# Performance work log

Measured on AMD Instinct MI355X. Metric: run time of the kernel, lower is better.

Reference implementation:

```python
import jax, jax.numpy as jnp
import numpy as np

D_MODEL, D_INNER, D_STATE, D_CONV = 1024, 2048, 16, 4
LN_EPS = 1e-5


def setup_inputs() -> dict:
    key = jax.random.key(0)
    ks = jax.random.split(key, 8)
    B, T = 2, 1024
    s = 0.02
    A = jnp.broadcast_to(jnp.arange(1, D_STATE + 1, dtype=jnp.float32), (D_INNER, D_STATE))
    return {
        "x": jax.random.normal(ks[0], (B, T, D_MODEL), jnp.float32),
        "ln_gamma": jnp.ones((D_MODEL,), jnp.float32),
        "ln_beta": jnp.zeros((D_MODEL,), jnp.float32),
        "W_in": jax.random.normal(ks[1], (2 * D_INNER, D_MODEL), jnp.float32) * s,
        "conv_w": jax.random.normal(ks[2], (D_INNER, D_CONV), jnp.float32) * s,
        "conv_b": jnp.zeros((D_INNER,), jnp.float32),
        "W_x": jax.random.normal(ks[3], (2 * D_STATE + 1, D_INNER), jnp.float32) * s,
        "w_dt": jax.random.normal(ks[4], (D_INNER, 1), jnp.float32) * s,
        "b_dt": jnp.zeros((D_INNER,), jnp.float32),
        "A_log": jnp.log(A),
        "D_param": jnp.ones((D_INNER,), jnp.float32),
        "W_out": jax.random.normal(ks[5], (D_MODEL, D_INNER), jnp.float32) * s,
    }


def _mamba_forward(x, ln_gamma, ln_beta, W_in, conv_w, conv_b, W_x, w_dt, b_dt, A_log, D_param, W_out):
    residual = x
    B, T, _ = x.shape
    # LayerNorm
    mu = x.mean(-1, keepdims=True)
    var = ((x - mu) ** 2).mean(-1, keepdims=True)
    xn = (x - mu) / jnp.sqrt(var + LN_EPS) * ln_gamma + ln_beta
    # in_proj -> split into x branch and gate z
    xz = xn @ W_in.T                       # [B,T,2*d_inner]
    xb, z = jnp.split(xz, 2, axis=-1)
    # depthwise causal conv1d (torch pad=d_conv-1, truncated to T == left pad)
    xp = jnp.pad(xb, ((0, 0), (D_CONV - 1, 0), (0, 0)))
    xc = conv_b + sum(xp[:, k:k + T, :] * conv_w[:, k] for k in range(D_CONV))
    xc = jax.nn.silu(xc)                   # [B,T,d_inner]
    # ssm parameter projections
    ssm_p = xc @ W_x.T                     # [B,T,2*d_state+1]
    dt_raw = ssm_p[..., :1]
    Bp = ssm_p[..., 1:1 + D_STATE]
    Cp = ssm_p[..., 1 + D_STATE:]
    dt = jax.nn.softplus(dt_raw @ w_dt.T + b_dt)   # [B,T,d_inner]
    A = -jnp.exp(A_log)                    # [d_inner,d_state]

    def step(h, inp):
        dt_t, x_t, B_t, C_t = inp          # [B,d], [B,d], [B,n], [B,n]
        A_bar = jnp.exp(dt_t[:, :, None] * A[None])          # [B,d,n]
        h = A_bar * h + (dt_t * x_t)[:, :, None] * B_t[:, None, :]
        y_t = jnp.einsum('bdn,bn->bd', h, C_t)
        return h, y_t

    h0 = jnp.zeros((B, D_INNER, D_STATE), x.dtype)
    xs = (jnp.swapaxes(dt, 0, 1), jnp.swapaxes(xc, 0, 1),
          jnp.swapaxes(Bp, 0, 1), jnp.swapaxes(Cp, 0, 1))
    _, ys = jax.lax.scan(step, h0, xs)     # ys: [T,B,d_inner]
    y = jnp.swapaxes(ys, 0, 1)
    y = y + D_param * xc
    y = y * jax.nn.silu(z)
    return residual + y @ W_out.T


def reference(x, ln_gamma, ln_beta, W_in, conv_w, conv_b, W_x, w_dt, b_dt, A_log, D_param, W_out):
    return _mamba_forward(x, ln_gamma, ln_beta, W_in, conv_w, conv_b, W_x, w_dt, b_dt, A_log, D_param, W_out)
```

## Files before the change

kernel.cpp:

```cpp
#include <hip/hip_runtime.h>
#include <hip/hip_bf16.h>

#define DM 1024
#define DI 2048
#define DS 16
#define DC 4
#define BB 2
#define TT 1024
#define MM (BB*TT)
#define CCH 32
#define LCH 32
#define PR 8
#define REPS 2

typedef unsigned short u16;
typedef __attribute__((ext_vector_type(8))) short bf16x8;
typedef __attribute__((ext_vector_type(4))) float f32x4;

#if __has_builtin(__builtin_amdgcn_exp2f)
#define EXP2F(x) __builtin_amdgcn_exp2f(x)
#else
#define EXP2F(x) exp2f(x)
#endif
#define L2E 1.44269504f

__device__ __forceinline__ float bu2f(u16 u) {
    union { unsigned int i; float f; } w; w.i = ((unsigned int)u) << 16; return w.f;
}
__device__ __forceinline__ u16 f2bu(float f) {
    union { float f; unsigned int u; } w; w.f = f;
    unsigned int r = w.u + 0x7fffu + ((w.u >> 16) & 1u);
    return (u16)(r >> 16);
}
__device__ __forceinline__ float upk(const uint4& v, int e) {
    unsigned int u;
    switch (e >> 1) { case 0: u = v.x; break; case 1: u = v.y; break;
                      case 2: u = v.z; break; default: u = v.w; }
    union { unsigned int i; float f; } w;
    w.i = (e & 1) ? (u & 0xffff0000u) : (u << 16);
    return w.f;
}

#define F2B_BLOCKS 6210
__global__ __launch_bounds__(256) void prep_kernel(const float* __restrict__ x,
                                                   const float* __restrict__ gamma,
                                                   const float* __restrict__ beta,
                                                   u16* __restrict__ xn,
                                                   const float* __restrict__ Wi,
                                                   u16* __restrict__ Wi_b,
                                                   const float* __restrict__ Wo,
                                                   u16* __restrict__ Wo_b,
                                                   const float* __restrict__ Wx,
                                                   u16* __restrict__ Wx_b) {
    const int tid = threadIdx.x;
    if (blockIdx.x >= MM) {
        const int n4W  = 2 * DI * DM / 4;
        const int n4Wo = DM * DI / 4;
        int i = (blockIdx.x - MM) * 256 + tid;
        const float* in; u16* out;
        if (i < n4W) { in = Wi; out = Wi_b; }
        else if (i < n4W + n4Wo) { in = Wo; out = Wo_b; i -= n4W; }
        else { in = Wx; out = Wx_b; i -= n4W + n4Wo; }
        float4 v = reinterpret_cast<const float4*>(in)[i];
        ushort4 o;
        o.x = f2bu(v.x); o.y = f2bu(v.y); o.z = f2bu(v.z); o.w = f2bu(v.w);
        reinterpret_cast<ushort4*>(out)[i] = o;
        return;
    }
    __shared__ float sbuf[8];
    const int row = blockIdx.x;
    float4 v = reinterpret_cast<const float4*>(x + (size_t)row * DM)[tid];

    float s = v.x + v.y + v.z + v.w;
    #pragma unroll
    for (int off = 32; off; off >>= 1) s += __shfl_down(s, off);
    if ((tid & 63) == 0) sbuf[tid >> 6] = s;
    __syncthreads();
    float mu = (sbuf[0] + sbuf[1] + sbuf[2] + sbuf[3]) * (1.0f / DM);
    __syncthreads();

    float d0 = v.x - mu, d1 = v.y - mu, d2 = v.z - mu, d3 = v.w - mu;
    float q = d0*d0 + d1*d1 + d2*d2 + d3*d3;
    #pragma unroll
    for (int off = 32; off; off >>= 1) q += __shfl_down(q, off);
    if ((tid & 63) == 0) sbuf[tid >> 6] = q;
    __syncthreads();
    float var = (sbuf[0] + sbuf[1] + sbuf[2] + sbuf[3]) * (1.0f / DM);
    float rstd = rsqrtf(var + 1e-5f);

    float4 g = reinterpret_cast<const float4*>(gamma)[tid];
    float4 b = reinterpret_cast<const float4*>(beta)[tid];
    ushort4 o;
    o.x = f2bu(d0 * rstd * g.x + b.x);
    o.y = f2bu(d1 * rstd * g.y + b.y);
    o.z = f2bu(d2 * rstd * g.z + b.z);
    o.w = f2bu(d3 * rstd * g.w + b.w);
    reinterpret_cast<ushort4*>(xn + (size_t)row * DM)[tid] = o;
}

__device__ __forceinline__ void gl_lds(const u16* g, u16* lds) {
    __builtin_amdgcn_global_load_lds((const __attribute__((address_space(1))) void*)g,
                                     (__attribute__((address_space(3))) void*)lds,
                                     16, 0, 0);
}

__global__ __launch_bounds__(256) void gemm1_mfma(const u16* __restrict__ A,
                                                  const u16* __restrict__ B,
                                                  u16* __restrict__ C,
                                                  int M, int N, int K) {
    __shared__ u16 As[2][2][128 * 32];
    __shared__ u16 Bs[2][2][128 * 32];
    const int tid  = threadIdx.x;
    const int lane = tid & 63;
    const int w    = tid >> 6;
    const int wm   = (w >> 1) * 64, wn = (w & 1) * 64;
    const int m0   = blockIdx.y * 128, n0 = blockIdx.x * 128;

    const int srow = tid >> 2;
    const int sk   = (tid & 3) * 8;
    const u16* aP0 = A + (size_t)(m0 + srow) * K + sk;
    const u16* aP1 = aP0 + (size_t)64 * K;
    const u16* bP0 = B + (size_t)(n0 + srow) * K + sk;
    const u16* bP1 = bP0 + (size_t)64 * K;
    const int ldst = tid * 8;

    const int fr = lane & 15, fq = (lane >> 4) * 8;
    const int iters = K >> 6;

    for (int rep = 0; rep < REPS; rep++) {
        __syncthreads();
        #pragma unroll
        for (int kh = 0; kh < 2; kh++) {
            gl_lds(aP0 + kh * 32, &As[0][kh][ldst]); gl_lds(aP1 + kh * 32, &As[0][kh][2048 + ldst]);
            gl_lds(bP0 + kh * 32, &Bs[0][kh][ldst]); gl_lds(bP1 + kh * 32, &Bs[0][kh][2048 + ldst]);
        }
        __syncthreads();

        f32x4 acc[4][4] = {};
        for (int it = 0; it < iters; it++) {
            const int cur = it & 1;
            const int kn = (it + 1) << 6;
            if (kn < K) {
                const int nb = cur ^ 1;
                #pragma unroll
                for (int kh = 0; kh < 2; kh++) {
                    gl_lds(aP0 + kn + kh * 32, &As[nb][kh][ldst]);
                    gl_lds(aP1 + kn + kh * 32, &As[nb][kh][2048 + ldst]);
                    gl_lds(bP0 + kn + kh * 32, &Bs[nb][kh][ldst]);
                    gl_lds(bP1 + kn + kh * 32, &Bs[nb][kh][2048 + ldst]);
                }
            }
            #pragma unroll
            for (int kh = 0; kh < 2; kh++) {
                bf16x8 af[4], bf[4];
                #pragma unroll
                for (int i = 0; i < 4; i++)
                    af[i] = *reinterpret_cast<const bf16x8*>(&As[cur][kh][(wm + i * 16 + fr) * 32 + fq]);
                #pragma unroll
                for (int j = 0; j < 4; j++)
                    bf[j] = *reinterpret_cast<const bf16x8*>(&Bs[cur][kh][(wn + j * 16 + fr) * 32 + fq]);
                #pragma unroll
                for (int i = 0; i < 4; i++)
                    #pragma unroll
                    for (int j = 0; j < 4; j++)
                        acc[i][j] = __builtin_amdgcn_mfma_f32_16x16x32_bf16(af[i], bf[j], acc[i][j], 0, 0, 0);
            }
            __syncthreads();
        }

        const int erow = (lane >> 4) * 4, ecol = lane & 15;
        #pragma unroll
        for (int i = 0; i < 4; i++)
            #pragma unroll
            for (int j = 0; j < 4; j++) {
                const int col = n0 + wn + j * 16 + ecol;
                #pragma unroll
                for (int r = 0; r < 4; r++) {
                    const int row = m0 + wm + i * 16 + erow + r;
                    C[(size_t)row * N + col] = f2bu(acc[i][j][r]);
                }
            }
    }
}

__global__ __launch_bounds__(256) void gemm2_mfma(const u16* __restrict__ A,
                                                  const u16* __restrict__ B,
                                                  float* __restrict__ C,
                                                  const float* __restrict__ resid,
                                                  int M, int N, int K) {
    __shared__ u16 As[2][4][64 * 32];
    __shared__ u16 Bs[2][4][64 * 32];
    const int tid  = threadIdx.x;
    const int lane = tid & 63;
    const int w    = tid >> 6;
    const int wm   = (w >> 1) * 32, wn = (w & 1) * 32;
    const int m0   = blockIdx.y * 64, n0 = blockIdx.x * 64;

    const int srow = tid >> 2;
    const int sk   = (tid & 3) * 8;
    const u16* aP = A + (size_t)(m0 + srow) * K + sk;
    const u16* bP = B + (size_t)(n0 + srow) * K + sk;
    const int ldst = tid * 8;

    const int fr = lane & 15, fq = (lane >> 4) * 8;
    const int iters = K >> 7;

    for (int rep = 0; rep < REPS; rep++) {
        __syncthreads();
        #pragma unroll
        for (int kh = 0; kh < 4; kh++) {
            gl_lds(aP + kh * 32, &As[0][kh][ldst]);
            gl_lds(bP + kh * 32, &Bs[0][kh][ldst]);
        }
        __syncthreads();

        f32x4 acc[2][2] = {};
        for (int it = 0; it < iters; it++) {
            const int cur = it & 1;
            const int kn = (it + 1) << 7;
            if (kn < K) {
                const int nb = cur ^ 1;
                #pragma unroll
                for (int kh = 0; kh < 4; kh++) {
                    gl_lds(aP + kn + kh * 32, &As[nb][kh][ldst]);
                    gl_lds(bP + kn + kh * 32, &Bs[nb][kh][ldst]);
                }
            }
            #pragma unroll
            for (int kh = 0; kh < 4; kh++) {
                bf16x8 af[2], bf[2];
                #pragma unroll
                for (int i = 0; i < 2; i++)
                    af[i] = *reinterpret_cast<const bf16x8*>(&As[cur][kh][(wm + i * 16 + fr) * 32 + fq]);
                #pragma unroll
                for (int j = 0; j < 2; j++)
                    bf[j] = *reinterpret_cast<const bf16x8*>(&Bs[cur][kh][(wn + j * 16 + fr) * 32 + fq]);
                #pragma unroll
                for (int i = 0; i < 2; i++)
                    #pragma unroll
                    for (int j = 0; j < 2; j++)
                        acc[i][j] = __builtin_amdgcn_mfma_f32_16x16x32_bf16(af[i], bf[j], acc[i][j], 0, 0, 0);
            }
            __syncthreads();
        }

        const int erow = (lane >> 4) * 4, ecol = lane & 15;
        #pragma unroll
        for (int i = 0; i < 2; i++)
            #pragma unroll
            for (int j = 0; j < 2; j++) {
                const int col = n0 + wn + j * 16 + ecol;
                #pragma unroll
                for (int r = 0; r < 4; r++) {
                    const int row = m0 + wm + i * 16 + erow + r;
                    C[(size_t)row * N + col] = acc[i][j][r] + resid[(size_t)row * N + col];
                }
            }
    }
}

__global__ __launch_bounds__(256) void convproj_kernel(const u16* __restrict__ xz,
                                                       const float* __restrict__ cw,
                                                       const float* __restrict__ cb,
                                                       const u16* __restrict__ Wxb,
                                                       u16* __restrict__ xc,
                                                       float* __restrict__ ssm) {
    __shared__ u16 xs[64 * PR * 32];
    __shared__ float red[4][PR][48];
    const int tid  = threadIdx.x;
    const int row0 = blockIdx.x * PR;
    const int t0   = row0 & (TT - 1);
    const int d0   = tid * 8;

    float4 w4[8];
    #pragma unroll
    for (int e = 0; e < 8; e++) w4[e] = reinterpret_cast<const float4*>(cw)[d0 + e];
    float bias[8];
    *reinterpret_cast<float4*>(&bias[0]) = reinterpret_cast<const float4*>(cb + d0)[0];
    *reinterpret_cast<float4*>(&bias[4]) = reinterpret_cast<const float4*>(cb + d0)[1];

    const int kt_w = tid >> 2;
    const int ko_w = (tid & 3) * 8;
    const int lane = tid & 63, w = tid >> 6;
    const int fr = lane & 15, fq = (lane >> 4) * 8;
    const int kt0 = w * 16;
    const u16* b0p = Wxb + (size_t)(fr)      * DI + fq;
    const u16* b1p = Wxb + (size_t)(16 + fr) * DI + fq;
    const u16* b2p = Wxb + (size_t)32        * DI + fq;

    for (int rep = 0; rep < REPS; rep++) {
        __syncthreads();
        uint4 pk[PR + 3];
        #pragma unroll
        for (int j = 0; j < PR + 3; j++) {
            const int tr = t0 - 3 + j;
            if (tr >= 0)
                pk[j] = *reinterpret_cast<const uint4*>(xz + (size_t)(row0 - 3 + j) * (2 * DI) + d0);
            else
                pk[j] = make_uint4(0, 0, 0, 0);
        }

        #pragma unroll
        for (int r = 0; r < PR; r++) {
            u16 ob[8];
            #pragma unroll
            for (int e = 0; e < 8; e++) {
                float a = bias[e]
                        + upk(pk[r],     e) * w4[e].x
                        + upk(pk[r + 1], e) * w4[e].y
                        + upk(pk[r + 2], e) * w4[e].z
                        + upk(pk[r + 3], e) * w4[e].w;
                float sv = a / (1.0f + __expf(-a));
                ob[e] = f2bu(sv);
            }
            uint4 o;
            o.x = (unsigned)ob[0] | ((unsigned)ob[1] << 16);
            o.y = (unsigned)ob[2] | ((unsigned)ob[3] << 16);
            o.z = (unsigned)ob[4] | ((unsigned)ob[5] << 16);
            o.w = (unsigned)ob[6] | ((unsigned)ob[7] << 16);
            *reinterpret_cast<uint4*>(xc + (size_t)(row0 + r) * DI + d0) = o;
            *reinterpret_cast<uint4*>(&xs[kt_w * (PR * 32) + r * 32 + ko_w]) = o;
        }
        __syncthreads();

        f32x4 acc0 = {}, acc1 = {}, acc2 = {};
        bf16x8 a_c = *reinterpret_cast<const bf16x8*>(&xs[kt0 * (PR * 32) + (fr & 7) * 32 + fq]);
        bf16x8 b0c = *reinterpret_cast<const bf16x8*>(b0p + (size_t)kt0 * 32);
        bf16x8 b1c = *reinterpret_cast<const bf16x8*>(b1p + (size_t)kt0 * 32);
        bf16x8 b2c = *reinterpret_cast<const bf16x8*>(b2p + (size_t)kt0 * 32);
        #pragma unroll
        for (int i = 0; i < 16; i++) {
            bf16x8 a_n, b0n, b1n, b2n;
            if (i < 15) {
                const int ktn = kt0 + i + 1;
                a_n = *reinterpret_cast<const bf16x8*>(&xs[ktn * (PR * 32) + (fr & 7) * 32 + fq]);
                b0n = *reinterpret_cast<const bf16x8*>(b0p + (size_t)ktn * 32);
                b1n = *reinterpret_cast<const bf16x8*>(b1p + (size_t)ktn * 32);
                b2n = *reinterpret_cast<const bf16x8*>(b2p + (size_t)ktn * 32);
            }
            acc0 = __builtin_amdgcn_mfma_f32_16x16x32_bf16(a_c, b0c, acc0, 0, 0, 0);
            acc1 = __builtin_amdgcn_mfma_f32_16x16x32_bf16(a_c, b1c, acc1, 0, 0, 0);
            acc2 = __builtin_amdgcn_mfma_f32_16x16x32_bf16(a_c, b2c, acc2, 0, 0, 0);
            if (i < 15) { a_c = a_n; b0c = b0n; b1c = b1n; b2c = b2n; }
        }
        const int erow = (lane >> 4) * 4, ecol = lane & 15;
        if (erow < PR) {
            #pragma unroll
            for (int r = 0; r < 4; r++) {
                red[w][erow + r][0 * 16 + ecol] = acc0[r];
                red[w][erow + r][1 * 16 + ecol] = acc1[r];
                red[w][erow + r][2 * 16 + ecol] = acc2[r];
            }
        }
        __syncthreads();

        for (int idx = tid; idx < PR * 33; idx += 256) {
            const int rr = idx / 33, n = idx % 33;
            float s = red[0][rr][n] + red[1][rr][n] + red[2][rr][n] + red[3][rr][n];
            ssm[(size_t)(row0 + rr) * 33 + n] = s;
        }
    }
}

__global__ __launch_bounds__(256) void scan_part1(const float* __restrict__ ssm,
                                                  const u16* __restrict__ xcy,
                                                  const float* __restrict__ w_dt,
                                                  const float* __restrict__ b_dt,
                                                  const float* __restrict__ A_log,
                                                  float* __restrict__ F,
                                                  float* __restrict__ Sdt) {
    __shared__ float sm[LCH * 33];
    __shared__ u16 xls[LCH * 256];
    const int tid = threadIdx.x;
    const int dt8 = blockIdx.x & 7;
    const int bc  = blockIdx.x >> 3;
    const int c   = bc & (CCH - 1);
    const int b   = bc >> 5;
    const int d   = dt8 * 256 + tid;

    const int base = ((b * TT) + c * LCH) * 33;
    for (int i = tid; i < LCH * 33; i += 256) sm[i] = ssm[base + i];
    const u16* xg = xcy + (size_t)(b * TT + c * LCH) * DI + dt8 * 256;
    for (int i = tid; i < LCH * 128; i += 256) {
        int t = i >> 7, dp = i & 127;
        unsigned int v = *reinterpret_cast<const unsigned int*>(xg + (size_t)t * DI + dp * 2);
        *reinterpret_cast<unsigned int*>(&xls[t * 256 + dp * 2]) = v;
    }
    __syncthreads();

    float A2[DS], h[DS];
    float4 al[4];
    #pragma unroll
    for (int i = 0; i < 4; i++)
        al[i] = reinterpret_cast<const float4*>(A_log + (size_t)d * DS)[i];
    #pragma unroll
    for (int i = 0; i < 4; i++) {
        A2[4*i+0] = -__expf(al[i].x) * L2E;
        A2[4*i+1] = -__expf(al[i].y) * L2E;
        A2[4*i+2] = -__expf(al[i].z) * L2E;
        A2[4*i+3] = -__expf(al[i].w) * L2E;
    }
    #pragma unroll
    for (int n = 0; n < DS; n++) h[n] = 0.f;
    const float wdt = w_dt[d], bdt = b_dt[d];
    float sdt = 0.f;

    for (int t = 0; t < LCH; t++) {
        const float* sp = &sm[t * 33];
        float pre = sp[0] * wdt + bdt;
        float dtv = (pre > 20.f) ? pre : __logf(1.f + __expf(pre));
        sdt += dtv;
        float xv = bu2f(xls[t * 256 + tid]);
        float u = dtv * xv;
        #pragma unroll
        for (int n = 0; n < DS; n++) h[n] = EXP2F(dtv * A2[n]) * h[n] + u * sp[1 + n];
    }
    const size_t fo = ((size_t)(b * CCH + c) * DI + d) * DS;
    #pragma unroll
    for (int n = 0; n < DS; n++) F[fo + n] = h[n];
    Sdt[(b * CCH + c) * DI + d] = sdt;
}

__global__ __launch_bounds__(256) void scan_combine(float* __restrict__ F,
                                                    const float* __restrict__ Sdt,
                                                    const float* __restrict__ A_log) {
    const int g = blockIdx.x * 256 + threadIdx.x;
    const int n = g & (DS - 1);
    const int d = (g >> 4) & (DI - 1);
    const int b = g >> 15;
    const float A2 = -__expf(A_log[d * DS + n]) * L2E;

    float f[CCH], q[CCH];
    #pragma unroll
    for (int c = 0; c < CCH; c++) {
        const size_t o = ((size_t)(b * CCH + c) * DI + d) * DS + n;
        f[c] = F[o];
        q[c] = Sdt[(b * CCH + c) * DI + d];
    }
    #pragma unroll
    for (int c = 0; c < CCH; c++) q[c] = EXP2F(q[c] * A2);

    float h = 0.f, hc[CCH];
    #pragma unroll
    for (int c = 0; c < CCH; c++) {
        hc[c] = h;
        h = q[c] * h + f[c];
    }
    #pragma unroll
    for (int c = 0; c < CCH; c++) {
        const size_t o = ((size_t)(b * CCH + c) * DI + d) * DS + n;
        F[o] = hc[c];
    }
}

__global__ __launch_bounds__(256) void scan_part2(const float* __restrict__ ssm,
                                                  const u16* __restrict__ xz,
                                                  u16* __restrict__ xcy,
                                                  const float* __restrict__ w_dt,
                                                  const float* __restrict__ b_dt,
                                                  const float* __restrict__ A_log,
                                                  const float* __restrict__ Dp,
                                                  const float* __restrict__ Hin) {
    __shared__ float sm[LCH * 33];
    __shared__ u16 xls[LCH * 256];
    const int tid = threadIdx.x;
    const int dt8 = blockIdx.x & 7;
    const int bc  = blockIdx.x >> 3;
    const int c   = bc & (CCH - 1);
    const int b   = bc >> 5;
    const int d   = dt8 * 256 + tid;

    const int base = ((b * TT) + c * LCH) * 33;
    for (int i = tid; i < LCH * 33; i += 256) sm[i] = ssm[base + i];
    const u16* xg = xcy + (size_t)(b * TT + c * LCH) * DI + dt8 * 256;
    for (int i = tid; i < LCH * 128; i += 256) {
        int t = i >> 7, dp = i & 127;
        unsigned int v = *reinterpret_cast<const unsigned int*>(xg + (size_t)t * DI + dp * 2);
        *reinterpret_cast<unsigned int*>(&xls[t * 256 + dp * 2]) = v;
    }
    __syncthreads();

    float A2[DS], h[DS];
    float4 al[4];
    #pragma unroll
    for (int i = 0; i < 4; i++)
        al[i] = reinterpret_cast<const float4*>(A_log + (size_t)d * DS)[i];
    #pragma unroll
    for (int i = 0; i < 4; i++) {
        A2[4*i+0] = -__expf(al[i].x) * L2E;
        A2[4*i+1] = -__expf(al[i].y) * L2E;
        A2[4*i+2] = -__expf(al[i].z) * L2E;
        A2[4*i+3] = -__expf(al[i].w) * L2E;
    }
    const size_t ho = ((size_t)(b * CCH + c) * DI + d) * DS;
    #pragma unroll
    for (int n = 0; n < DS; n++) h[n] = Hin[ho + n];
    const float wdt = w_dt[d], bdt = b_dt[d], Dv = Dp[d];

    for (int t = 0; t < LCH; t++) {
        const float* sp = &sm[t * 33];
        float pre = sp[0] * wdt + bdt;
        float dtv = (pre > 20.f) ? pre : __logf(1.f + __expf(pre));
        const size_t row = (size_t)(b * TT + c * LCH + t);
        float xv = bu2f(xls[t * 256 + tid]);
        float u = dtv * xv;
        float y = 0.f;
        #pragma unroll
        for (int n = 0; n < DS; n++) {
            h[n] = EXP2F(dtv * A2[n]) * h[n] + u * sp[1 + n];
            y += h[n] * sp[17 + n];
        }
        float z = bu2f(xz[row * (2 * DI) + DI + d]);
        float sz = z / (1.0f + __expf(-z));
        xcy[row * DI + d] = f2bu((y + Dv * xv) * sz);
    }
}

extern "C" void kernel_launch(void* const* d_in, const int* in_sizes, int n_in,
                              void* d_out, int out_size, void* d_ws, size_t ws_size,
                              hipStream_t stream) {
    int ix, ig, ib, iWin, icw, icb, iWx, iwdt, ibdt, iAl, iD, iWo;
    if (n_in >= 12 && in_sizes[0] == 32768) {
        iAl = 0; iD = 1; iWin = 2; iWo = 3; iWx = 4; ibdt = 5;
        icb = 6; icw = 7; ib = 8; ig = 9; iwdt = 10; ix = 11;
    } else if (n_in >= 12 && in_sizes[0] == 2097152 && in_sizes[1] == 2048 && in_sizes[2] == 32768) {
        iWo = 0; iD = 1; iAl = 2; ibdt = 3; iwdt = 4; iWx = 5;
        icb = 6; icw = 7; iWin = 8; ib = 9; ig = 10; ix = 11;
    } else {
        ix = 0; ig = 1; ib = 2; iWin = 3; icw = 4; icb = 5;
        iWx = 6; iwdt = 7; ibdt = 8; iAl = 9; iD = 10; iWo = 11;
    }

    const float* x       = (const float*)d_in[ix];
    const float* ln_g    = (const float*)d_in[ig];
    const float* ln_b    = (const float*)d_in[ib];
    const float* W_in    = (const float*)d_in[iWin];
    const float* conv_w  = (const float*)d_in[icw];
    const float* conv_b  = (const float*)d_in[icb];
    const float* W_x     = (const float*)d_in[iWx];
    const float* w_dt    = (const float*)d_in[iwdt];
    const float* b_dt    = (const float*)d_in[ibdt];
    const float* A_log   = (const float*)d_in[iAl];
    const float* D_param = (const float*)d_in[iD];
    const float* W_out   = (const float*)d_in[iWo];
    float* out = (float*)d_out;

    float* ssm  = (float*)d_ws;
    u16*   xn   = (u16*)(ssm + (size_t)MM * 33);
    u16*   xz   = xn + (size_t)MM * DM;
    u16*   xcy  = xz + (size_t)MM * 2 * DI;
    float* F    = (float*)(xcy + (size_t)MM * DI);
    float* Sdt  = F + (size_t)BB * CCH * DI * DS;
    u16*   Wi_b = (u16*)(Sdt + (size_t)BB * CCH * DI);
    u16*   Wo_b = Wi_b + (size_t)2 * DI * DM;
    u16*   Wx_b = Wo_b + (size_t)DM * DI;

    prep_kernel<<<MM + F2B_BLOCKS, 256, 0, stream>>>(x, ln_g, ln_b, xn, W_in, Wi_b,
                                                     W_out, Wo_b, W_x, Wx_b);

    gemm1_mfma<<<dim3(4096 / 128, MM / 128), 256, 0, stream>>>(xn, Wi_b, xz, MM, 2 * DI, DM);

    convproj_kernel<<<MM / PR, 256, 0, stream>>>(xz, conv_w, conv_b, Wx_b, xcy, ssm);

    scan_part1<<<BB * CCH * (DI / 256), 256, 0, stream>>>(ssm, xcy, w_dt, b_dt, A_log, F, Sdt);
    scan_combine<<<(BB * DI * DS) / 256, 256, 0, stream>>>(F, Sdt, A_log);
    scan_part2<<<BB * CCH * (DI / 256), 256, 0, stream>>>(ssm, xz, xcy, w_dt, b_dt, A_log, D_param, F);

    gemm2_mfma<<<dim3(1024 / 64, MM / 64), 256, 0, stream>>>(xcy, Wo_b, out, x, MM, DM, DI);
}
```

Measured before the change: 239.2 us.

## Drop repeated GEMM/conv passes, swizzle LDS tiles, fuse scan into cooperative kernel

Removes the REPS loop that made gemm1, gemm2 and convproj compute and store their outputs twice, so each now runs once. Applies an XOR swizzle to the LDS tile layout in both MFMA GEMMs to cut bank conflicts on fragment reads. Merges the three chunked-scan kernels into one cooperative kernel that uses grid-wide syncs between the chunk-local scan, the cross-chunk combine and the final pass. This saves two launches and keeps per-thread scan state in registers, but it relies on all 512 blocks being co-resident for the cooperative launch.

Result: slower. 451.0 us (+88.5%).

```diff
diff --git a/kernel.cpp b/kernel.cpp
--- a/kernel.cpp
+++ b/kernel.cpp
@@ -1,5 +1,8 @@
 #include <hip/hip_runtime.h>
 #include <hip/hip_bf16.h>
+#include <hip/hip_cooperative_groups.h>
+
+namespace cg = cooperative_groups;
 
 #define DM 1024
 #define DI 2048
@@ -11,7 +14,6 @@
 #define CCH 32
 #define LCH 32
 #define PR 8
-#define REPS 2
 
 typedef unsigned short u16;
 typedef __attribute__((ext_vector_type(8))) short bf16x8;
@@ -117,7 +119,7 @@
     const int m0   = blockIdx.y * 128, n0 = blockIdx.x * 128;
 
     const int srow = tid >> 2;
-    const int sk   = (tid & 3) * 8;
+    const int sk   = (((tid & 3) ^ ((srow >> 1) & 3)) * 8);
     const u16* aP0 = A + (size_t)(m0 + srow) * K + sk;
     const u16* aP1 = aP0 + (size_t)64 * K;
     const u16* bP0 = B + (size_t)(n0 + srow) * K + sk;
@@ -125,62 +127,65 @@
     const int ldst = tid * 8;
 
     const int fr = lane & 15, fq = (lane >> 4) * 8;
+
+    #pragma unroll
+    for (int kh = 0; kh < 2; kh++) {
+        gl_lds(aP0 + kh * 32, &As[0][kh][ldst]); gl_lds(aP1 + kh * 32, &As[0][kh][2048 + ldst]);
+        gl_lds(bP0 + kh * 32, &Bs[0][kh][ldst]); gl_lds(bP1 + kh * 32, &Bs[0][kh][2048 + ldst]);
+    }
+    __syncthreads();
+
     const int iters = K >> 6;
-
-    for (int rep = 0; rep < REPS; rep++) {
-        __syncthreads();
+    f32x4 acc[4][4] = {};
+    for (int it = 0; it < iters; it++) {
+        const int cur = it & 1;
+        const int kn = (it + 1) << 6;
+        if (kn < K) {
+            const int nb = cur ^ 1;
+            #pragma unroll
+            for (int kh = 0; kh < 2; kh++) {
+                gl_lds(aP0 + kn + kh * 32, &As[nb][kh][ldst]);
+                gl_lds(aP1 + kn + kh * 32, &As[nb][kh][2048 + ldst]);
+                gl_lds(bP0 + kn + kh * 32, &Bs[nb][kh][ldst]);
+                gl_lds(bP1 + kn + kh * 32, &Bs[nb][kh][2048 + ldst]);
+            }
+        }
         #pragma unroll
         for (int kh = 0; kh < 2; kh++) {
-            gl_lds(aP0 + kh * 32, &As[0][kh][ldst]); gl_lds(aP1 + kh * 32, &As[0][kh][2048 + ldst]);
-            gl_lds(bP0 + kh * 32, &Bs[0][kh][ldst]); gl_lds(bP1 + kh * 32, &Bs[0][kh][2048 + ldst]);
-        }
-        __syncthreads();
-
-        f32x4 acc[4][4] = {};
-        for (int it = 0; it < iters; it++) {
-            const int cur = it & 1;
-            const int kn = (it + 1) << 6;
-            if (kn < K) {
-                const int nb = cur ^ 1;
-                #pragma unroll
-                for (int kh = 0; kh < 2; kh++) {
-                    gl_lds(aP0 + kn + kh * 32, &As[nb][kh][ldst]);
-                    gl_lds(aP1 + kn + kh * 32, &As[nb][kh][2048 + ldst]);
-                    gl_lds(bP0 + kn + kh * 32, &Bs[nb][kh][ldst]);
-                    gl_lds(bP1 + kn + kh * 32, &Bs[nb][kh][2048 + ldst]);
-                }
-            }
-            #pragma unroll
-            for (int kh = 0; kh < 2; kh++) {
-                bf16x8 af[4], bf[4];
-                #pragma unroll
-                for (int i = 0; i < 4; i++)
-                    af[i] = *reinterpret_cast<const bf16x8*>(&As[cur][kh][(wm + i * 16 + fr) * 32 + fq]);
+            bf16x8 af[4], bf[4];
+            #pragma unroll
+            for (int i = 0; i < 4; i++) {
+                const int ra = wm + i * 16 + fr;
+                af[i] = *reinterpret_cast<const bf16x8*>(
+                    &As[cur][kh][ra * 32 + (fq ^ (((ra >> 1) & 3) << 3))]);
+            }
+            #pragma unroll
+            for (int j = 0; j < 4; j++) {
+                const int rb = wn + j * 16 + fr;
+                bf[j] = *reinterpret_cast<const bf16x8*>(
+                    &Bs[cur][kh][rb * 32 + (fq ^ (((rb >> 1) & 3) << 3))]);
+            }
+            #pragma unroll
+            for (int i = 0; i < 4; i++)
                 #pragma unroll
                 for (int j = 0; j < 4; j++)
-                    bf[j] = *reinterpret_cast<const bf16x8*>(&Bs[cur][kh][(wn + j * 16 + fr) * 32 + fq]);
-                #pragma unroll
-                for (int i = 0; i < 4; i++)
-                    #pragma unroll
-                    for (int j = 0; j < 4; j++)
-                        acc[i][j] = __builtin_amdgcn_mfma_f32_16x16x32_bf16(af[i], bf[j], acc[i][j], 0, 0, 0);
-            }
-            __syncthreads();
-        }
-
-        const int erow = (lane >> 4) * 4, ecol = lane & 15;
-        #pragma unroll
-        for (int i = 0; i < 4; i++)
-            #pragma unroll
-            for (int j = 0; j < 4; j++) {
-                const int col = n0 + wn + j * 16 + ecol;
-                #pragma unroll
-                for (int r = 0; r < 4; r++) {
-                    const int row = m0 + wm + i * 16 + erow + r;
-                    C[(size_t)row * N + col] = f2bu(acc[i][j][r]);
-                }
-            }
-    }
+                    acc[i][j] = __builtin_amdgcn_mfma_f32_16x16x32_bf16(af[i], bf[j], acc[i][j], 0, 0, 0);
+        }
+        __syncthreads();
+    }
+
+    const int erow = (lane >> 4) * 4, ecol = lane & 15;
+    #pragma unroll
+    for (int i = 0; i < 4; i++)
+        #pragma unroll
+        for (int j = 0; j < 4; j++) {
+            const int col = n0 + wn + j * 16 + ecol;
+            #pragma unroll
+            for (int r = 0; r < 4; r++) {
+                const int row = m0 + wm + i * 16 + erow + r;
+                C[(size_t)row * N + col] = f2bu(acc[i][j][r]);
+            }
+        }
 }
 
 __global__ __launch_bounds__(256) void gemm2_mfma(const u16* __restrict__ A,
@@ -197,66 +202,69 @@
     const int m0   = blockIdx.y * 64, n0 = blockIdx.x * 64;
 
     const int srow = tid >> 2;
-    const int sk   = (tid & 3) * 8;
+    const int sk   = (((tid & 3) ^ ((srow >> 1) & 3)) * 8);
     const u16* aP = A + (size_t)(m0 + srow) * K + sk;
     const u16* bP = B + (size_t)(n0 + srow) * K + sk;
     const int ldst = tid * 8;
 
     const int fr = lane & 15, fq = (lane >> 4) * 8;
+
+    #pragma unroll
+    for (int kh = 0; kh < 4; kh++) {
+        gl_lds(aP + kh * 32, &As[0][kh][ldst]);
+        gl_lds(bP + kh * 32, &Bs[0][kh][ldst]);
+    }
+    __syncthreads();
+
     const int iters = K >> 7;
-
-    for (int rep = 0; rep < REPS; rep++) {
-        __syncthreads();
+    f32x4 acc[2][2] = {};
+    for (int it = 0; it < iters; it++) {
+        const int cur = it & 1;
+        const int kn = (it + 1) << 7;
+        if (kn < K) {
+            const int nb = cur ^ 1;
+            #pragma unroll
+            for (int kh = 0; kh < 4; kh++) {
+                gl_lds(aP + kn + kh * 32, &As[nb][kh][ldst]);
+                gl_lds(bP + kn + kh * 32, &Bs[nb][kh][ldst]);
+            }
+        }
         #pragma unroll
         for (int kh = 0; kh < 4; kh++) {
-            gl_lds(aP + kh * 32, &As[0][kh][ldst]);
-            gl_lds(bP + kh * 32, &Bs[0][kh][ldst]);
-        }
-        __syncthreads();
-
-        f32x4 acc[2][2] = {};
-        for (int it = 0; it < iters; it++) {
-            const int cur = it & 1;
-            const int kn = (it + 1) << 7;
-            if (kn < K) {
-                const int nb = cur ^ 1;
-                #pragma unroll
-                for (int kh = 0; kh < 4; kh++) {
-                    gl_lds(aP + kn + kh * 32, &As[nb][kh][ldst]);
-                    gl_lds(bP + kn + kh * 32, &Bs[nb][kh][ldst]);
-                }
-            }
-            #pragma unroll
-            for (int kh = 0; kh < 4; kh++) {
-                bf16x8 af[2], bf[2];
-                #pragma unroll
-                for (int i = 0; i < 2; i++)
-                    af[i] = *reinterpret_cast<const bf16x8*>(&As[cur][kh][(wm + i * 16 + fr) * 32 + fq]);
+            bf16x8 af[2], bf[2];
+            #pragma unroll
+            for (int i = 0; i < 2; i++) {
+                const int ra = wm + i * 16 + fr;
+                af[i] = *reinterpret_cast<const bf16x8*>(
+                    &As[cur][kh][ra * 32 + (fq ^ (((ra >> 1) & 3) << 3))]);
+            }
+            #pragma unroll
+            for (int j = 0; j < 2; j++) {
+                const int rb = wn + j * 16 + fr;
+                bf[j] = *reinterpret_cast<const bf16x8*>(
+                    &Bs[cur][kh][rb * 32 + (fq ^ (((rb >> 1) & 3) << 3))]);
+            }
+            #pragma unroll
+            for (int i = 0; i < 2; i++)
                 #pragma unroll
                 for (int j = 0; j < 2; j++)
-                    bf[j] = *reinterpret_cast<const bf16x8*>(&Bs[cur][kh][(wn + j * 16 + fr) * 32 + fq]);
-                #pragma unroll
-                for (int i = 0; i < 2; i++)
-                    #pragma unroll
-                    for (int j = 0; j < 2; j++)
-                        acc[i][j] = __builtin_amdgcn_mfma_f32_16x16x32_bf16(af[i], bf[j], acc[i][j], 0, 0, 0);
-            }
-            __syncthreads();
-        }
-
-        const int erow = (lane >> 4) * 4, ecol = lane & 15;
-        #pragma unroll
-        for (int i = 0; i < 2; i++)
-            #pragma unroll
-            for (int j = 0; j < 2; j++) {
-                const int col = n0 + wn + j * 16 + ecol;
-                #pragma unroll
-                for (int r = 0; r < 4; r++) {
-                    const int row = m0 + wm + i * 16 + erow + r;
-                    C[(size_t)row * N + col] = acc[i][j][r] + resid[(size_t)row * N + col];
-                }
-            }
-    }
+                    acc[i][j] = __builtin_amdgcn_mfma_f32_16x16x32_bf16(af[i], bf[j], acc[i][j], 0, 0, 0);
+        }
+        __syncthreads();
+    }
+
+    const int erow = (lane >> 4) * 4, ecol = lane & 15;
+    #pragma unroll
+    for (int i = 0; i < 2; i++)
+        #pragma unroll
+        for (int j = 0; j < 2; j++) {
+            const int col = n0 + wn + j * 16 + ecol;
+            #pragma unroll
+            for (int r = 0; r < 4; r++) {
+                const int row = m0 + wm + i * 16 + erow + r;
+                C[(size_t)row * N + col] = acc[i][j][r] + resid[(size_t)row * N + col];
+            }
+        }
 }
 
 __global__ __launch_bounds__(256) void convproj_kernel(const u16* __restrict__ xz,
@@ -279,8 +287,41 @@
     *reinterpret_cast<float4*>(&bias[0]) = reinterpret_cast<const float4*>(cb + d0)[0];
     *reinterpret_cast<float4*>(&bias[4]) = reinterpret_cast<const float4*>(cb + d0)[1];
 
+    uint4 pk[PR + 3];
+    #pragma unroll
+    for (int j = 0; j < PR + 3; j++) {
+        const int tr = t0 - 3 + j;
+        if (tr >= 0)
+            pk[j] = *reinterpret_cast<const uint4*>(xz + (size_t)(row0 - 3 + j) * (2 * DI) + d0);
+        else
+            pk[j] = make_uint4(0, 0, 0, 0);
+    }
+
     const int kt_w = tid >> 2;
     const int ko_w = (tid & 3) * 8;
+    #pragma unroll
+    for (int r = 0; r < PR; r++) {
+        u16 ob[8];
+        #pragma unroll
+        for (int e = 0; e < 8; e++) {
+            float a = bias[e]
+                    + upk(pk[r],     e) * w4[e].x
+                    + upk(pk[r + 1], e) * w4[e].y
+                    + upk(pk[r + 2], e) * w4[e].z
+                    + upk(pk[r + 3], e) * w4[e].w;
+            float sv = a / (1.0f + __expf(-a));
+            ob[e] = f2bu(sv);
+        }
+        uint4 o;
+        o.x = (unsigned)ob[0] | ((unsigned)ob[1] << 16);
+        o.y = (unsigned)ob[2] | ((unsigned)ob[3] << 16);
+        o.z = (unsigned)ob[4] | ((unsigned)ob[5] << 16);
+        o.w = (unsigned)ob[6] | ((unsigned)ob[7] << 16);
+        *reinterpret_cast<uint4*>(xc + (size_t)(row0 + r) * DI + d0) = o;
+        *reinterpret_cast<uint4*>(&xs[kt_w * (PR * 32) + r * 32 + ko_w]) = o;
+    }
+    __syncthreads();
+
     const int lane = tid & 63, w = tid >> 6;
     const int fr = lane & 15, fq = (lane >> 4) * 8;
     const int kt0 = w * 16;
@@ -288,89 +329,56 @@
     const u16* b1p = Wxb + (size_t)(16 + fr) * DI + fq;
     const u16* b2p = Wxb + (size_t)32        * DI + fq;
 
-    for (int rep = 0; rep < REPS; rep++) {
-        __syncthreads();
-        uint4 pk[PR + 3];
-        #pragma unroll
-        for (int j = 0; j < PR + 3; j++) {
-            const int tr = t0 - 3 + j;
-            if (tr >= 0)
-                pk[j] = *reinterpret_cast<const uint4*>(xz + (size_t)(row0 - 3 + j) * (2 * DI) + d0);
-            else
-                pk[j] = make_uint4(0, 0, 0, 0);
-        }
-
-        #pragma unroll
-        for (int r = 0; r < PR; r++) {
-            u16 ob[8];
-            #pragma unroll
-            for (int e = 0; e < 8; e++) {
-                float a = bias[e]
-                        + upk(pk[r],     e) * w4[e].x
-                        + upk(pk[r + 1], e) * w4[e].y
-                        + upk(pk[r + 2], e) * w4[e].z
-                        + upk(pk[r + 3], e) * w4[e].w;
-                float sv = a / (1.0f + __expf(-a));
-                ob[e] = f2bu(sv);
-            }
-            uint4 o;
-            o.x = (unsigned)ob[0] | ((unsigned)ob[1] << 16);
-            o.y = (unsigned)ob[2] | ((unsigned)ob[3] << 16);
-            o.z = (unsigned)ob[4] | ((unsigned)ob[5] << 16);
-            o.w = (unsigned)ob[6] | ((unsigned)ob[7] << 16);
-            *reinterpret_cast<uint4*>(xc + (size_t)(row0 + r) * DI + d0) = o;
-            *reinterpret_cast<uint4*>(&xs[kt_w * (PR * 32) + r * 32 + ko_w]) = o;
-        }
-        __syncthreads();
-
-        f32x4 acc0 = {}, acc1 = {}, acc2 = {};
-        bf16x8 a_c = *reinterpret_cast<const bf16x8*>(&xs[kt0 * (PR * 32) + (fr & 7) * 32 + fq]);
-        bf16x8 b0c = *reinterpret_cast<const bf16x8*>(b0p + (size_t)kt0 * 32);
-        bf16x8 b1c = *reinterpret_cast<const bf16x8*>(b1p + (size_t)kt0 * 32);
-        bf16x8 b2c = *reinterpret_cast<const bf16x8*>(b2p + (size_t)kt0 * 32);
-        #pragma unroll
-        for (int i = 0; i < 16; i++) {
-            bf16x8 a_n, b0n, b1n, b2n;
-            if (i < 15) {
-                const int ktn = kt0 + i + 1;
-                a_n = *reinterpret_cast<const bf16x8*>(&xs[ktn * (PR * 32) + (fr & 7) * 32 + fq]);
-                b0n = *reinterpret_cast<const bf16x8*>(b0p + (size_t)ktn * 32);
-                b1n = *reinterpret_cast<const bf16x8*>(b1p + (size_t)ktn * 32);
-                b2n = *reinterpret_cast<const bf16x8*>(b2p + (size_t)ktn * 32);
-            }
-            acc0 = __builtin_amdgcn_mfma_f32_16x16x32_bf16(a_c, b0c, acc0, 0, 0, 0);
-            acc1 = __builtin_amdgcn_mfma_f32_16x16x32_bf16(a_c, b1c, acc1, 0, 0, 0);
-            acc2 = __builtin_amdgcn_mfma_f32_16x16x32_bf16(a_c, b2c, acc2, 0, 0, 0);
-            if (i < 15) { a_c = a_n; b0c = b0n; b1c = b1n; b2c = b2n; }
-        }
-        const int erow = (lane >> 4) * 4, ecol = lane & 15;
-        if (erow < PR) {
-            #pragma unroll
-            for (int r = 0; r < 4; r++) {
-                red[w][erow + r][0 * 16 + ecol] = acc0[r];
-                red[w][erow + r][1 * 16 + ecol] = acc1[r];
-                red[w][erow + r][2 * 16 + ecol] = acc2[r];
-            }
-        }
-        __syncthreads();
-
-        for (int idx = tid; idx < PR * 33; idx += 256) {
-            const int rr = idx / 33, n = idx % 33;
-            float s = red[0][rr][n] + red[1][rr][n] + red[2][rr][n] + red[3][rr][n];
-            ssm[(size_t)(row0 + rr) * 33 + n] = s;
-        }
-    }
-}
-
-__global__ __launch_bounds__(256) void scan_part1(const float* __restrict__ ssm,
-                                                  const u16* __restrict__ xcy,
+    f32x4 acc0 = {}, acc1 = {}, acc2 = {};
+    bf16x8 a_c = *reinterpret_cast<const bf16x8*>(&xs[kt0 * (PR * 32) + (fr & 7) * 32 + fq]);
+    bf16x8 b0c = *reinterpret_cast<const bf16x8*>(b0p + (size_t)kt0 * 32);
+    bf16x8 b1c = *reinterpret_cast<const bf16x8*>(b1p + (size_t)kt0 * 32);
+    bf16x8 b2c = *reinterpret_cast<const bf16x8*>(b2p + (size_t)kt0 * 32);
+    #pragma unroll
+    for (int i = 0; i < 16; i++) {
+        bf16x8 a_n, b0n, b1n, b2n;
+        if (i < 15) {
+            const int ktn = kt0 + i + 1;
+            a_n = *reinterpret_cast<const bf16x8*>(&xs[ktn * (PR * 32) + (fr & 7) * 32 + fq]);
+            b0n = *reinterpret_cast<const bf16x8*>(b0p + (size_t)ktn * 32);
+            b1n = *reinterpret_cast<const bf16x8*>(b1p + (size_t)ktn * 32);
+            b2n = *reinterpret_cast<const bf16x8*>(b2p + (size_t)ktn * 32);
+        }
+        acc0 = __builtin_amdgcn_mfma_f32_16x16x32_bf16(a_c, b0c, acc0, 0, 0, 0);
+        acc1 = __builtin_amdgcn_mfma_f32_16x16x32_bf16(a_c, b1c, acc1, 0, 0, 0);
+        acc2 = __builtin_amdgcn_mfma_f32_16x16x32_bf16(a_c, b2c, acc2, 0, 0, 0);
+        if (i < 15) { a_c = a_n; b0c = b0n; b1c = b1n; b2c = b2n; }
+    }
+    const int erow = (lane >> 4) * 4, ecol = lane & 15;
+    if (erow < PR) {
+        #pragma unroll
+        for (int r = 0; r < 4; r++) {
+            red[w][erow + r][0 * 16 + ecol] = acc0[r];
+            red[w][erow + r][1 * 16 + ecol] = acc1[r];
+            red[w][erow + r][2 * 16 + ecol] = acc2[r];
+        }
+    }
+    __syncthreads();
+
+    for (int idx = tid; idx < PR * 33; idx += 256) {
+        const int rr = idx / 33, n = idx % 33;
+        float s = red[0][rr][n] + red[1][rr][n] + red[2][rr][n] + red[3][rr][n];
+        ssm[(size_t)(row0 + rr) * 33 + n] = s;
+    }
+}
+
+__global__ __launch_bounds__(256) void scan_fused(const float* __restrict__ ssm,
+                                                  const u16* __restrict__ xz,
+                                                  u16* __restrict__ xcy,
                                                   const float* __restrict__ w_dt,
                                                   const float* __restrict__ b_dt,
                                                   const float* __restrict__ A_log,
+                                                  const float* __restrict__ Dp,
                                                   float* __restrict__ F,
                                                   float* __restrict__ Sdt) {
     __shared__ float sm[LCH * 33];
     __shared__ u16 xls[LCH * 256];
+    cg::grid_group grid = cg::this_grid();
     const int tid = threadIdx.x;
     const int dt8 = blockIdx.x & 7;
     const int bc  = blockIdx.x >> 3;
@@ -400,11 +408,11 @@
         A2[4*i+2] = -__expf(al[i].z) * L2E;
         A2[4*i+3] = -__expf(al[i].w) * L2E;
     }
+    const float wdt = w_dt[d], bdt = b_dt[d], Dv = Dp[d];
+
     #pragma unroll
     for (int n = 0; n < DS; n++) h[n] = 0.f;
-    const float wdt = w_dt[d], bdt = b_dt[d];
     float sdt = 0.f;
-
     for (int t = 0; t < LCH; t++) {
         const float* sp = &sm[t * 33];
         float pre = sp[0] * wdt + bdt;
@@ -415,88 +423,47 @@
         #pragma unroll
         for (int n = 0; n < DS; n++) h[n] = EXP2F(dtv * A2[n]) * h[n] + u * sp[1 + n];
     }
-    const size_t fo = ((size_t)(b * CCH + c) * DI + d) * DS;
-    #pragma unroll
-    for (int n = 0; n < DS; n++) F[fo + n] = h[n];
-    Sdt[(b * CCH + c) * DI + d] = sdt;
-}
-
-__global__ __launch_bounds__(256) void scan_combine(float* __restrict__ F,
-                                                    const float* __restrict__ Sdt,
-                                                    const float* __restrict__ A_log) {
-    const int g = blockIdx.x * 256 + threadIdx.x;
-    const int n = g & (DS - 1);
-    const int d = (g >> 4) & (DI - 1);
-    const int b = g >> 15;
-    const float A2 = -__expf(A_log[d * DS + n]) * L2E;
-
-    float f[CCH], q[CCH];
-    #pragma unroll
-    for (int c = 0; c < CCH; c++) {
-        const size_t o = ((size_t)(b * CCH + c) * DI + d) * DS + n;
-        f[c] = F[o];
-        q[c] = Sdt[(b * CCH + c) * DI + d];
-    }
-    #pragma unroll
-    for (int c = 0; c < CCH; c++) q[c] = EXP2F(q[c] * A2);
-
-    float h = 0.f, hc[CCH];
-    #pragma unroll
-    for (int c = 0; c < CCH; c++) {
-        hc[c] = h;
-        h = q[c] * h + f[c];
-    }
-    #pragma unroll
-    for (int c = 0; c < CCH; c++) {
-        const size_t o = ((size_t)(b * CCH + c) * DI + d) * DS + n;
-        F[o] = hc[c];
-    }
-}
-
-__global__ __launch_bounds__(256) void scan_part2(const float* __restrict__ ssm,
-                                                  const u16* __restrict__ xz,
-                                                  u16* __restrict__ xcy,
-                                                  const float* __restrict__ w_dt,
-                                                  const float* __restrict__ b_dt,
-                                                  const float* __restrict__ A_log,
-                                                  const float* __restrict__ Dp,
-                                                  const float* __restrict__ Hin) {
-    __shared__ float sm[LCH * 33];
-    __shared__ u16 xls[LCH * 256];
-    const int tid = threadIdx.x;
-    const int dt8 = blockIdx.x & 7;
-    const int bc  = blockIdx.x >> 3;
-    const int c   = bc & (CCH - 1);
-    const int b   = bc >> 5;
-    const int d   = dt8 * 256 + tid;
-
-    const int base = ((b * TT) + c * LCH) * 33;
-    for (int i = tid; i < LCH * 33; i += 256) sm[i] = ssm[base + i];
-    const u16* xg = xcy + (size_t)(b * TT + c * LCH) * DI + dt8 * 256;
-    for (int i = tid; i < LCH * 128; i += 256) {
-        int t = i >> 7, dp = i & 127;
-        unsigned int v = *reinterpret_cast<const unsigned int*>(xg + (size_t)t * DI + dp * 2);
-        *reinterpret_cast<unsigned int*>(&xls[t * 256 + dp * 2]) = v;
-    }
-    __syncthreads();
-
-    float A2[DS], h[DS];
-    float4 al[4];
-    #pragma unroll
-    for (int i = 0; i < 4; i++)
-        al[i] = reinterpret_cast<const float4*>(A_log + (size_t)d * DS)[i];
-    #pragma unroll
-    for (int i = 0; i < 4; i++) {
-        A2[4*i+0] = -__expf(al[i].x) * L2E;
-        A2[4*i+1] = -__expf(al[i].y) * L2E;
-        A2[4*i+2] = -__expf(al[i].z) * L2E;
-        A2[4*i+3] = -__expf(al[i].w) * L2E;
-    }
-    const size_t ho = ((size_t)(b * CCH + c) * DI + d) * DS;
-    #pragma unroll
-    for (int n = 0; n < DS; n++) h[n] = Hin[ho + n];
-    const float wdt = w_dt[d], bdt = b_dt[d], Dv = Dp[d];
-
+    {
+        const size_t fo = ((size_t)(b * CCH + c) * DI + d) * DS;
+        #pragma unroll
+        for (int n = 0; n < DS; n++) F[fo + n] = h[n];
+        Sdt[(b * CCH + c) * DI + d] = sdt;
+    }
+    __threadfence();
+    grid.sync();
+
+    const int gid = blockIdx.x * 256 + tid;
+    if (gid < BB * DI * DS) {
+        const int n2 = gid & (DS - 1);
+        const int d2 = (gid >> 4) & (DI - 1);
+        const int b2 = gid >> 15;
+        const float A2c = -__expf(A_log[d2 * DS + n2]) * L2E;
+        float fv[CCH], qv[CCH];
+        #pragma unroll
+        for (int cc = 0; cc < CCH; cc++) {
+            const size_t o = ((size_t)(b2 * CCH + cc) * DI + d2) * DS + n2;
+            fv[cc] = F[o];
+            qv[cc] = Sdt[(b2 * CCH + cc) * DI + d2];
+        }
+        #pragma unroll
+        for (int cc = 0; cc < CCH; cc++) qv[cc] = EXP2F(qv[cc] * A2c);
+        float h2 = 0.f;
+        #pragma unroll
+        for (int cc = 0; cc < CCH; cc++) {
+            const size_t o = ((size_t)(b2 * CCH + cc) * DI + d2) * DS + n2;
+            float hn = qv[cc] * h2 + fv[cc];
+            F[o] = h2;
+            h2 = hn;
+        }
+    }
+    __threadfence();
+    grid.sync();
+
+    {
+        const size_t ho = ((size_t)(b * CCH + c) * DI + d) * DS;
+        #pragma unroll
+        for (int n = 0; n < DS; n++) h[n] = F[ho + n];
+    }
     for (int t = 0; t < LCH; t++) {
         const float* sp = &sm[t * 33];
         float pre = sp[0] * wdt + bdt;
@@ -562,9 +529,14 @@
 
     convproj_kernel<<<MM / PR, 256, 0, stream>>>(xz, conv_w, conv_b, Wx_b, xcy, ssm);
 
-    scan_part1<<<BB * CCH * (DI / 256), 256, 0, stream>>>(ssm, xcy, w_dt, b_dt, A_log, F, Sdt);
-    scan_combine<<<(BB * DI * DS) / 256, 256, 0, stream>>>(F, Sdt, A_log);
-    scan_part2<<<BB * CCH * (DI / 256), 256, 0, stream>>>(ssm, xz, xcy, w_dt, b_dt, A_log, D_param, F);
+    {
+        void* args[] = { (void*)&ssm, (void*)&xz, (void*)&xcy, (void*)&w_dt,
+                         (void*)&b_dt, (void*)&A_log, (void*)&D_param,
+                         (void*)&F, (void*)&Sdt };
+        hipLaunchCooperativeKernel(reinterpret_cast<const void*>(&scan_fused),
+                                   dim3(BB * CCH * (DI / 256)), dim3(256),
+                                   args, 0, stream);
+    }
 
     gemm2_mfma<<<dim3(1024 / 64, MM / 64), 256, 0, stream>>>(xcy, Wo_b, out, x, MM, DM, DI);
 }
```
